# Optimization experiments

Hardware: AMD Instinct MI355X
Metric: run time of the kernel (lower is better)

Reference implementation:

```python
import jax, jax.numpy as jnp
import numpy as np

G, M, K = 4096, 50, 30          # graphs, nodes per graph, sort-pool k
H, NUM_LAYERS, F_IN = 32, 3, 128
DEG = 8
N = G * M
E = N * DEG
D_LAT = H * NUM_LAYERS + 1       # 97 = conv1d kernel/stride
DENSE_DIM = (((K - 2) // 2 + 1) - 5 + 1) * 32  # 352


def setup_inputs() -> dict:
    key = jax.random.key(0)
    ks = jax.random.split(key, 14)
    x = jax.random.normal(ks[0], (N, F_IN), dtype=jnp.float32)
    # graph-local random edges so each subgraph is self-contained
    offs = (jnp.arange(E, dtype=jnp.int32) // (M * DEG)) * M
    src = jax.random.randint(ks[1], (E,), 0, M, dtype=jnp.int32) + offs
    dst = jax.random.randint(ks[2], (E,), 0, M, dtype=jnp.int32) + offs
    edge_index = jnp.stack([src, dst])
    batch = jnp.repeat(jnp.arange(G, dtype=jnp.int32), M)

    def lin(k, i, o):
        return (jax.random.normal(k, (i, o), dtype=jnp.float32) / np.sqrt(i)).astype(jnp.float32)

    W0, b0 = lin(ks[3], F_IN, H), jnp.zeros((H,), jnp.float32)
    W1, b1 = lin(ks[4], H, H), jnp.zeros((H,), jnp.float32)
    W2, b2 = lin(ks[5], H, H), jnp.zeros((H,), jnp.float32)
    W3, b3 = lin(ks[6], H, 1), jnp.zeros((1,), jnp.float32)
    C1w = (jax.random.normal(ks[7], (16, 1, D_LAT)) / np.sqrt(D_LAT)).astype(jnp.float32)
    C1b = jnp.zeros((16,), jnp.float32)
    C2w = (jax.random.normal(ks[8], (32, 16, 5)) / np.sqrt(16 * 5)).astype(jnp.float32)
    C2b = jnp.zeros((32,), jnp.float32)
    L1w, L1b = lin(ks[9], DENSE_DIM, 128), jnp.zeros((128,), jnp.float32)
    L2w, L2b = lin(ks[10], 128, 1), jnp.zeros((1,), jnp.float32)
    return {"x": x, "edge_index": edge_index, "batch": batch,
            "W0": W0, "b0": b0, "W1": W1, "b1": b1, "W2": W2, "b2": b2,
            "W3": W3, "b3": b3, "C1w": C1w, "C1b": C1b, "C2w": C2w, "C2b": C2b,
            "L1w": L1w, "L1b": L1b, "L2w": L2w, "L2b": L2b}


def _gcn_norm(edge_index, n):
    # add self loops, symmetric normalization (PyG GCNConv default)
    loop = jnp.arange(n, dtype=edge_index.dtype)
    src = jnp.concatenate([edge_index[0], loop])
    dst = jnp.concatenate([edge_index[1], loop])
    deg = jax.ops.segment_sum(jnp.ones_like(dst, dtype=jnp.float32), dst, num_segments=n)
    dinv = jnp.where(deg > 0, deg ** -0.5, 0.0)
    return src, dst, dinv[src] * dinv[dst]


def _gcn_conv(h, W, b, src, dst, norm, n):
    h = h @ W                                    # [N, out]
    msg = h[src] * norm[:, None]                 # gather + weight
    return jax.ops.segment_sum(msg, dst, num_segments=n) + b


def reference(x, edge_index, batch, W0, b0, W1, b1, W2, b2, W3, b3,
              C1w, C1b, C2w, C2b, L1w, L1b, L2w, L2b):
    n = x.shape[0]
    src, dst, norm = _gcn_norm(edge_index, n)
    h1 = jnp.tanh(_gcn_conv(x, W0, b0, src, dst, norm, n))
    h2 = jnp.tanh(_gcn_conv(h1, W1, b1, src, dst, norm, n))
    h3 = jnp.tanh(_gcn_conv(h2, W2, b2, src, dst, norm, n))
    h4 = jnp.tanh(_gcn_conv(h3, W3, b3, src, dst, norm, n))
    lat = jnp.concatenate([h1, h2, h3, h4], axis=-1)      # [N, 97]
    # global_sort_pool: graphs are contiguous equal-size blocks (batch = arange(G).repeat(M)),
    # sort nodes within each graph by last channel, descending, keep top K
    xd = lat.reshape(G, M, D_LAT)
    order = jnp.argsort(-xd[..., -1], axis=1)             # [G, M]
    xs = jnp.take_along_axis(xd, order[..., None], axis=1)[:, :K]  # [G, K, 97]
    # Conv1d(1,16,97,stride=97) on [G,1,K*97] == per-slot linear over the 97 latent dims
    z = jnp.einsum('gtd,cd->gct', xs, C1w[:, 0, :]) + C1b[None, :, None]  # [G,16,K]
    z = jax.nn.relu(z)
    z = z.reshape(G, 16, K // 2, 2).max(axis=-1)          # MaxPool1d(2,2) -> [G,16,15]
    z = jax.lax.conv_general_dilated(z, C2w, window_strides=(1,), padding='VALID',
                                     dimension_numbers=('NCH', 'OIH', 'NCH'))
    z = jax.nn.relu(z + C2b[None, :, None])               # [G,32,11]
    z = z.reshape(G, -1)                                  # [G,352]
    z = jax.nn.relu(z @ L1w + L1b)
    # dropout: eval mode (identity)
    return z @ L2w + L2b                                  # [G,1]
```

## Files before the change

kernel.cpp:

```cpp
#include <hip/hip_runtime.h>
#include <math.h>

#define NG 4096
#define M 50
#define KTOP 30
#define H 32
#define F_IN 128
#define EPG 400
#define PADE 552
#define E_TOTAL (NG * EPG)
#define DLAT 97
#define LATS 100
#define NTHREADS 256

__device__ __forceinline__ float fast_tanh(float x) {
    x = fminf(fmaxf(x, -15.f), 15.f);
    float e = __expf(2.f * x);
    return 1.f - 2.f / (e + 1.f);
}

template <int KIN>
__device__ __forceinline__ void gcn_matmul(const float* hin, int istride,
                                           const float* __restrict__ W,
                                           float (*tb)[H], int tid) {
    const int j = tid & 31, iset = tid >> 5;
    float acc[7];
    int rows[7];
#pragma unroll
    for (int r = 0; r < 7; r++) {
        acc[r] = 0.f;
        int i = iset + r * 8;
        rows[r] = (i >= M) ? (M - 1) : i;
    }
#pragma unroll 2
    for (int k4 = 0; k4 < KIN / 4; k4++) {
        const float w0 = W[(4 * k4 + 0) * H + j];
        const float w1 = W[(4 * k4 + 1) * H + j];
        const float w2 = W[(4 * k4 + 2) * H + j];
        const float w3 = W[(4 * k4 + 3) * H + j];
#pragma unroll
        for (int r = 0; r < 7; r++) {
            const float4 xv = *(const float4*)(hin + rows[r] * istride + 4 * k4);
            acc[r] += xv.x * w0 + xv.y * w1 + xv.z * w2 + xv.w * w3;
        }
    }
#pragma unroll
    for (int r = 0; r < 7; r++) {
        int i = iset + r * 8;
        if (i < M) tb[i][j] = acc[r];
    }
}

__device__ __forceinline__ void gcn_agg(const float (*tbuf)[H], const float* __restrict__ b,
                                        float (*lat)[LATS], int col0,
                                        const float* dinv, const unsigned short* csr_off,
                                        const unsigned char* csr_src, const float* csr_nrm,
                                        int tid) {
    const int j = tid & 31, iset = tid >> 5;
    for (int i = iset; i < M; i += 8) {
        float acc = tbuf[i][j] * dinv[i] * dinv[i];
        int e0 = csr_off[i], e1 = csr_off[i + 1];
        for (int e = e0; e < e1; e += 4) {
            unsigned sp = *(const unsigned*)(csr_src + e);
            float4 nr = *(const float4*)(csr_nrm + e);
            acc += tbuf[sp & 255][j] * nr.x;
            acc += tbuf[(sp >> 8) & 255][j] * nr.y;
            acc += tbuf[(sp >> 16) & 255][j] * nr.z;
            acc += tbuf[sp >> 24][j] * nr.w;
        }
        lat[i][col0 + j] = fast_tanh(acc + b[j]);
    }
}

__global__ __launch_bounds__(NTHREADS, 4)
void dgcnn_kernel(const float* __restrict__ x, const int* __restrict__ eidx,
                  const float* __restrict__ W0, const float* __restrict__ b0,
                  const float* __restrict__ W1, const float* __restrict__ b1,
                  const float* __restrict__ W2, const float* __restrict__ b2,
                  const float* __restrict__ W3, const float* __restrict__ b3,
                  const float* __restrict__ C1w, const float* __restrict__ C1b,
                  const float* __restrict__ C2w, const float* __restrict__ C2b,
                  const float* __restrict__ L1w, const float* __restrict__ L1b,
                  const float* __restrict__ L2w, const float* __restrict__ L2b,
                  float* __restrict__ out) {
    __shared__ __align__(16) float lat[M][LATS];
    __shared__ float tbuf[M][H];
    __shared__ __align__(16) float csr_nrm[PADE];
    __shared__ unsigned char csr_src[PADE];
    __shared__ unsigned short csr_off[M + 2];
    __shared__ int   degi[M];
    __shared__ float dinv[M];
    __shared__ struct Post {
        float pbuf[16][15];
        union {
            struct { float z1[16][KTOP]; unsigned char ord[52]; } a;
            struct { float z2[352]; float d1[128]; } b;
        } u;
    } post;

    const int g = blockIdx.x;
    const int tid = threadIdx.x;
    const int nbase = g * M;
    const int ebase = g * EPG;
    const float* xg = x + (size_t)nbase * F_IN;

    if (tid < M) degi[tid] = 1;
    for (int idx = tid; idx < PADE; idx += NTHREADS) {
        csr_nrm[idx] = 0.f;
        csr_src[idx] = 0;
    }
    __syncthreads();
    for (int e = tid; e < EPG; e += NTHREADS) {
        int d = eidx[E_TOTAL + ebase + e] - nbase;
        atomicAdd(&degi[d], 1);
    }
    __syncthreads();
    if (tid < M) dinv[tid] = rsqrtf((float)degi[tid]);
    if (tid < 64) {
        int cnt  = (tid < M) ? (degi[tid] - 1) : 0;
        int cntp = (cnt + 3) & ~3;
        int incl = cntp;
#pragma unroll
        for (int off = 1; off < 64; off <<= 1) {
            int nv = __shfl_up(incl, off);
            if (tid >= off) incl += nv;
        }
        if (tid < M) {
            csr_off[tid] = (unsigned short)(incl - cntp);
            degi[tid] = incl - cntp;
        }
        if (tid == M - 1) csr_off[M] = (unsigned short)incl;
    }
    __syncthreads();
    for (int e = tid; e < EPG; e += NTHREADS) {
        int s = eidx[ebase + e] - nbase;
        int d = eidx[E_TOTAL + ebase + e] - nbase;
        float nr = dinv[s] * dinv[d];
        int pos = atomicAdd(&degi[d], 1);
        csr_src[pos] = (unsigned char)s;
        csr_nrm[pos] = nr;
    }
    __syncthreads();

    gcn_matmul<F_IN>(xg, F_IN, W0, tbuf, tid);
    __syncthreads();
    gcn_agg(tbuf, b0, lat, 0, dinv, csr_off, csr_src, csr_nrm, tid);
    __syncthreads();
    gcn_matmul<H>(&lat[0][0], LATS, W1, tbuf, tid);
    __syncthreads();
    gcn_agg(tbuf, b1, lat, 32, dinv, csr_off, csr_src, csr_nrm, tid);
    __syncthreads();
    gcn_matmul<H>(&lat[0][32], LATS, W2, tbuf, tid);
    __syncthreads();
    gcn_agg(tbuf, b2, lat, 64, dinv, csr_off, csr_src, csr_nrm, tid);
    __syncthreads();
    if (tid < M) {
        float acc = 0.f;
        for (int k = 0; k < H; k++) acc += lat[tid][64 + k] * W3[k];
        tbuf[tid][0] = acc;
    }
    __syncthreads();
    if (tid < M) {
        float acc = tbuf[tid][0] * dinv[tid] * dinv[tid];
        int e0 = csr_off[tid], e1 = csr_off[tid + 1];
        for (int e = e0; e < e1; e += 4) {
            unsigned sp = *(const unsigned*)(csr_src + e);
            float4 nr = *(const float4*)(csr_nrm + e);
            acc += tbuf[sp & 255][0] * nr.x + tbuf[(sp >> 8) & 255][0] * nr.y
                 + tbuf[(sp >> 16) & 255][0] * nr.z + tbuf[sp >> 24][0] * nr.w;
        }
        lat[tid][96] = tanhf(acc + b3[0]);
    }
    __syncthreads();

    if (tid < M) {
        float v = lat[tid][96];
        int r = 0;
        for (int jj = 0; jj < M; jj++) {
            float vj = lat[jj][96];
            r += (vj > v) || (vj == v && jj < tid);
        }
        post.u.a.ord[r] = (unsigned char)tid;
    }
    __syncthreads();

    for (int idx = tid; idx < 16 * KTOP; idx += NTHREADS) {
        int t = idx >> 4, c = idx & 15;
        const float* row = lat[post.u.a.ord[t]];
        float acc = 0.f;
        for (int d = 0; d < DLAT; d++) acc += row[d] * C1w[c * DLAT + d];
        acc += C1b[c];
        post.u.a.z1[c][t] = fmaxf(acc, 0.f);
    }
    __syncthreads();

    for (int idx = tid; idx < 16 * 15; idx += NTHREADS) {
        int c = idx / 15, t = idx - c * 15;
        post.pbuf[c][t] = fmaxf(post.u.a.z1[c][2 * t], post.u.a.z1[c][2 * t + 1]);
    }
    __syncthreads();

    for (int idx = tid; idx < 352; idx += NTHREADS) {
        int o = idx / 11, t = idx - o * 11;
        float acc = C2b[o];
        for (int i = 0; i < 16; i++) {
#pragma unroll
            for (int k = 0; k < 5; k++)
                acc += post.pbuf[i][t + k] * C2w[(o * 16 + i) * 5 + k];
        }
        post.u.b.z2[idx] = fmaxf(acc, 0.f);
    }
    __syncthreads();

    if (tid < 128) {
        float acc = L1b[tid];
        for (int f = 0; f < 352; f++) acc += post.u.b.z2[f] * L1w[f * 128 + tid];
        post.u.b.d1[tid] = fmaxf(acc, 0.f);
    }
    __syncthreads();

    if (tid < 64) {
        float v = post.u.b.d1[tid] * L2w[tid]
                + post.u.b.d1[tid + 64] * L2w[tid + 64];
#pragma unroll
        for (int off = 32; off >= 1; off >>= 1)
            v += __shfl_down(v, off);
        if (tid == 0) out[g] = v + L2b[0];
    }
}

extern "C" void kernel_launch(void* const* d_in, const int* in_sizes, int n_in,
                              void* d_out, int out_size, void* d_ws, size_t ws_size,
                              hipStream_t stream) {
    const float* x    = (const float*)d_in[0];
    const int*   eidx = (const int*)d_in[1];
    dgcnn_kernel<<<NG, NTHREADS, 0, stream>>>(
        x, eidx,
        (const float*)d_in[3],  (const float*)d_in[4],
        (const float*)d_in[5],  (const float*)d_in[6],
        (const float*)d_in[7],  (const float*)d_in[8],
        (const float*)d_in[9],  (const float*)d_in[10],
        (const float*)d_in[11], (const float*)d_in[12],
        (const float*)d_in[13], (const float*)d_in[14],
        (const float*)d_in[15], (const float*)d_in[16],
        (const float*)d_in[17], (const float*)d_in[18],
        (float*)d_out);
}
```

Baseline: 425.7 us.

## Pre-transpose weights into workspace for vectorized loads and split dense layer

Adds a small prep kernel that transposes W0/W1/W2 and L1w and pads C1w to 100 columns in the workspace, so the main kernel can read weights as float4 rows. The conv1 dot product, the GCN matmuls and the dense layer now use float4 loads from both shared memory and global memory. The dense layer is split across all 256 threads as two halves that are then reduced, and L2 is folded into that reduction. tbuf is overlapped in a union with the post-processing buffers to save shared memory. The cost is an extra kernel launch per call, and the lat padding columns must be zeroed.

```diff
diff --git a/kernel.cpp b/kernel.cpp
--- a/kernel.cpp
+++ b/kernel.cpp
@@ -13,17 +13,49 @@
 #define LATS 100
 #define NTHREADS 256
 
+#define WS_WT0 0
+#define WS_WT1 4096
+#define WS_WT2 5120
+#define WS_C1P 6144
+#define WS_L1T 7744
+#define WS_TOTAL 52800
+
 __device__ __forceinline__ float fast_tanh(float x) {
     x = fminf(fmaxf(x, -15.f), 15.f);
     float e = __expf(2.f * x);
     return 1.f - 2.f / (e + 1.f);
 }
 
+__global__ void prep_kernel(const float* __restrict__ W0, const float* __restrict__ W1,
+                            const float* __restrict__ W2, const float* __restrict__ C1w,
+                            const float* __restrict__ L1w, float* __restrict__ ws) {
+    const int tid = blockIdx.x * blockDim.x + threadIdx.x;
+    const int nthr = gridDim.x * blockDim.x;
+    for (int idx = tid; idx < 4096; idx += nthr) {
+        int j = idx >> 7, k = idx & 127;
+        ws[WS_WT0 + idx] = W0[k * 32 + j];
+    }
+    for (int idx = tid; idx < 1024; idx += nthr) {
+        int j = idx >> 5, k = idx & 31;
+        ws[WS_WT1 + idx] = W1[k * 32 + j];
+        ws[WS_WT2 + idx] = W2[k * 32 + j];
+    }
+    for (int idx = tid; idx < 1600; idx += nthr) {
+        int c = idx / 100, d = idx - c * 100;
+        ws[WS_C1P + idx] = (d < DLAT) ? C1w[c * DLAT + d] : 0.f;
+    }
+    for (int idx = tid; idx < 45056; idx += nthr) {
+        int j = idx / 352, f = idx - j * 352;
+        ws[WS_L1T + idx] = L1w[f * 128 + j];
+    }
+}
+
 template <int KIN>
 __device__ __forceinline__ void gcn_matmul(const float* hin, int istride,
-                                           const float* __restrict__ W,
+                                           const float* __restrict__ Wt,
                                            float (*tb)[H], int tid) {
     const int j = tid & 31, iset = tid >> 5;
+    const float* wrow = Wt + j * KIN;
     float acc[7];
     int rows[7];
 #pragma unroll
@@ -34,14 +66,11 @@
     }
 #pragma unroll 2
     for (int k4 = 0; k4 < KIN / 4; k4++) {
-        const float w0 = W[(4 * k4 + 0) * H + j];
-        const float w1 = W[(4 * k4 + 1) * H + j];
-        const float w2 = W[(4 * k4 + 2) * H + j];
-        const float w3 = W[(4 * k4 + 3) * H + j];
+        const float4 wv = *(const float4*)(wrow + 4 * k4);
 #pragma unroll
         for (int r = 0; r < 7; r++) {
             const float4 xv = *(const float4*)(hin + rows[r] * istride + 4 * k4);
-            acc[r] += xv.x * w0 + xv.y * w1 + xv.z * w2 + xv.w * w3;
+            acc[r] += xv.x * wv.x + xv.y * wv.y + xv.z * wv.z + xv.w * wv.w;
         }
     }
 #pragma unroll
@@ -74,29 +103,31 @@
 
 __global__ __launch_bounds__(NTHREADS, 4)
 void dgcnn_kernel(const float* __restrict__ x, const int* __restrict__ eidx,
-                  const float* __restrict__ W0, const float* __restrict__ b0,
-                  const float* __restrict__ W1, const float* __restrict__ b1,
-                  const float* __restrict__ W2, const float* __restrict__ b2,
+                  const float* __restrict__ ws,
+                  const float* __restrict__ b0, const float* __restrict__ b1,
+                  const float* __restrict__ b2,
                   const float* __restrict__ W3, const float* __restrict__ b3,
-                  const float* __restrict__ C1w, const float* __restrict__ C1b,
+                  const float* __restrict__ C1b,
                   const float* __restrict__ C2w, const float* __restrict__ C2b,
-                  const float* __restrict__ L1w, const float* __restrict__ L1b,
+                  const float* __restrict__ L1b,
                   const float* __restrict__ L2w, const float* __restrict__ L2b,
                   float* __restrict__ out) {
     __shared__ __align__(16) float lat[M][LATS];
-    __shared__ float tbuf[M][H];
+    __shared__ __align__(16) union TU {
+        float tbuf[M][H];
+        struct {
+            float pbuf[16][15];
+            union {
+                struct { float z1[16][KTOP]; unsigned char ord[52]; } a;
+                struct { float z2[352]; float red[256]; } b;
+            } u;
+        } post;
+    } tu;
     __shared__ __align__(16) float csr_nrm[PADE];
     __shared__ unsigned char csr_src[PADE];
     __shared__ unsigned short csr_off[M + 2];
     __shared__ int   degi[M];
     __shared__ float dinv[M];
-    __shared__ struct Post {
-        float pbuf[16][15];
-        union {
-            struct { float z1[16][KTOP]; unsigned char ord[52]; } a;
-            struct { float z2[352]; float d1[128]; } b;
-        } u;
-    } post;
 
     const int g = blockIdx.x;
     const int tid = threadIdx.x;
@@ -109,6 +140,7 @@
         csr_nrm[idx] = 0.f;
         csr_src[idx] = 0;
     }
+    if (tid < 3 * M) lat[tid / 3][DLAT + tid % 3] = 0.f;
     __syncthreads();
     for (int e = tid; e < EPG; e += NTHREADS) {
         int d = eidx[E_TOTAL + ebase + e] - nbase;
@@ -142,32 +174,32 @@
     }
     __syncthreads();
 
-    gcn_matmul<F_IN>(xg, F_IN, W0, tbuf, tid);
-    __syncthreads();
-    gcn_agg(tbuf, b0, lat, 0, dinv, csr_off, csr_src, csr_nrm, tid);
-    __syncthreads();
-    gcn_matmul<H>(&lat[0][0], LATS, W1, tbuf, tid);
-    __syncthreads();
-    gcn_agg(tbuf, b1, lat, 32, dinv, csr_off, csr_src, csr_nrm, tid);
-    __syncthreads();
-    gcn_matmul<H>(&lat[0][32], LATS, W2, tbuf, tid);
-    __syncthreads();
-    gcn_agg(tbuf, b2, lat, 64, dinv, csr_off, csr_src, csr_nrm, tid);
+    gcn_matmul<F_IN>(xg, F_IN, ws + WS_WT0, tu.tbuf, tid);
+    __syncthreads();
+    gcn_agg(tu.tbuf, b0, lat, 0, dinv, csr_off, csr_src, csr_nrm, tid);
+    __syncthreads();
+    gcn_matmul<H>(&lat[0][0], LATS, ws + WS_WT1, tu.tbuf, tid);
+    __syncthreads();
+    gcn_agg(tu.tbuf, b1, lat, 32, dinv, csr_off, csr_src, csr_nrm, tid);
+    __syncthreads();
+    gcn_matmul<H>(&lat[0][32], LATS, ws + WS_WT2, tu.tbuf, tid);
+    __syncthreads();
+    gcn_agg(tu.tbuf, b2, lat, 64, dinv, csr_off, csr_src, csr_nrm, tid);
     __syncthreads();
     if (tid < M) {
         float acc = 0.f;
         for (int k = 0; k < H; k++) acc += lat[tid][64 + k] * W3[k];
-        tbuf[tid][0] = acc;
+        tu.tbuf[tid][0] = acc;
     }
     __syncthreads();
     if (tid < M) {
-        float acc = tbuf[tid][0] * dinv[tid] * dinv[tid];
+        float acc = tu.tbuf[tid][0] * dinv[tid] * dinv[tid];
         int e0 = csr_off[tid], e1 = csr_off[tid + 1];
         for (int e = e0; e < e1; e += 4) {
             unsigned sp = *(const unsigned*)(csr_src + e);
             float4 nr = *(const float4*)(csr_nrm + e);
-            acc += tbuf[sp & 255][0] * nr.x + tbuf[(sp >> 8) & 255][0] * nr.y
-                 + tbuf[(sp >> 16) & 255][0] * nr.z + tbuf[sp >> 24][0] * nr.w;
+            acc += tu.tbuf[sp & 255][0] * nr.x + tu.tbuf[(sp >> 8) & 255][0] * nr.y
+                 + tu.tbuf[(sp >> 16) & 255][0] * nr.z + tu.tbuf[sp >> 24][0] * nr.w;
         }
         lat[tid][96] = tanhf(acc + b3[0]);
     }
@@ -180,23 +212,28 @@
             float vj = lat[jj][96];
             r += (vj > v) || (vj == v && jj < tid);
         }
-        post.u.a.ord[r] = (unsigned char)tid;
+        tu.post.u.a.ord[r] = (unsigned char)tid;
     }
     __syncthreads();
 
     for (int idx = tid; idx < 16 * KTOP; idx += NTHREADS) {
         int t = idx >> 4, c = idx & 15;
-        const float* row = lat[post.u.a.ord[t]];
+        const float4* row = (const float4*)lat[tu.post.u.a.ord[t]];
+        const float4* cw  = (const float4*)(ws + WS_C1P + c * LATS);
         float acc = 0.f;
-        for (int d = 0; d < DLAT; d++) acc += row[d] * C1w[c * DLAT + d];
-        acc += C1b[c];
-        post.u.a.z1[c][t] = fmaxf(acc, 0.f);
+#pragma unroll 5
+        for (int q = 0; q < LATS / 4; q++) {
+            float4 rv = row[q], wv = cw[q];
+            acc += rv.x * wv.x + rv.y * wv.y + rv.z * wv.z + rv.w * wv.w;
+        }
+        tu.post.u.a.z1[c][t] = fmaxf(acc + C1b[c], 0.f);
     }
     __syncthreads();
 
     for (int idx = tid; idx < 16 * 15; idx += NTHREADS) {
         int c = idx / 15, t = idx - c * 15;
-        post.pbuf[c][t] = fmaxf(post.u.a.z1[c][2 * t], post.u.a.z1[c][2 * t + 1]);
+        tu.post.pbuf[c][t] = fmaxf(tu.post.u.a.z1[c][2 * t],
+                                   tu.post.u.a.z1[c][2 * t + 1]);
     }
     __syncthreads();
 
@@ -206,22 +243,31 @@
         for (int i = 0; i < 16; i++) {
 #pragma unroll
             for (int k = 0; k < 5; k++)
-                acc += post.pbuf[i][t + k] * C2w[(o * 16 + i) * 5 + k];
-        }
-        post.u.b.z2[idx] = fmaxf(acc, 0.f);
-    }
-    __syncthreads();
-
-    if (tid < 128) {
-        float acc = L1b[tid];
-        for (int f = 0; f < 352; f++) acc += post.u.b.z2[f] * L1w[f * 128 + tid];
-        post.u.b.d1[tid] = fmaxf(acc, 0.f);
-    }
-    __syncthreads();
-
+                acc += tu.post.pbuf[i][t + k] * C2w[(o * 16 + i) * 5 + k];
+        }
+        tu.post.u.b.z2[idx] = fmaxf(acc, 0.f);
+    }
+    __syncthreads();
+
+    {
+        int jj = tid & 127, half = tid >> 7;
+        const float4* lw = (const float4*)(ws + WS_L1T + jj * 352 + half * 176);
+        const float4* zz = (const float4*)(tu.post.u.b.z2 + half * 176);
+        float acc = (half == 0) ? L1b[jj] : 0.f;
+#pragma unroll 4
+        for (int q = 0; q < 44; q++) {
+            float4 zv = zz[q], wv = lw[q];
+            acc += zv.x * wv.x + zv.y * wv.y + zv.z * wv.z + zv.w * wv.w;
+        }
+        tu.post.u.b.red[tid] = acc;
+    }
+    __syncthreads();
+    if (tid < 128)
+        tu.post.u.b.red[tid] = fmaxf(tu.post.u.b.red[tid] + tu.post.u.b.red[tid + 128],
+                                     0.f) * L2w[tid];
+    __syncthreads();
     if (tid < 64) {
-        float v = post.u.b.d1[tid] * L2w[tid]
-                + post.u.b.d1[tid + 64] * L2w[tid + 64];
+        float v = tu.post.u.b.red[tid] + tu.post.u.b.red[tid + 64];
 #pragma unroll
         for (int off = 32; off >= 1; off >>= 1)
             v += __shfl_down(v, off);
@@ -234,15 +280,19 @@
                               hipStream_t stream) {
     const float* x    = (const float*)d_in[0];
     const int*   eidx = (const int*)d_in[1];
+    float* ws = (float*)d_ws;
+    prep_kernel<<<64, 256, 0, stream>>>(
+        (const float*)d_in[3],  (const float*)d_in[5],
+        (const float*)d_in[7],  (const float*)d_in[11],
+        (const float*)d_in[15], ws);
     dgcnn_kernel<<<NG, NTHREADS, 0, stream>>>(
-        x, eidx,
-        (const float*)d_in[3],  (const float*)d_in[4],
-        (const float*)d_in[5],  (const float*)d_in[6],
-        (const float*)d_in[7],  (const float*)d_in[8],
+        x, eidx, ws,
+        (const float*)d_in[4],  (const float*)d_in[6],
+        (const float*)d_in[8],
         (const float*)d_in[9],  (const float*)d_in[10],
-        (const float*)d_in[11], (const float*)d_in[12],
+        (const float*)d_in[12],
         (const float*)d_in[13], (const float*)d_in[14],
-        (const float*)d_in[15], (const float*)d_in[16],
+        (const float*)d_in[16],
         (const float*)d_in[17], (const float*)d_in[18],
         (float*)d_out);
 }
```

New measurement: 488.9 us. 14.9% more time.

## Overlap first GCN matmul with CSR build and software-pipeline row loads

Applied to the files above, without the earlier changes.

The first-layer matmul over x is moved up so it runs between the degree-count atomics and the CSR construction. Its global loads then overlap with edge processing instead of waiting behind two extra barriers. Inside gcn_matmul, the float4 row loads for the next k-step are prefetched into registers while the current step computes (double buffering). The launch bound is lowered from 4 to 3 blocks per SM so the extra registers fit, which risks lower occupancy.

```diff
diff --git a/kernel.cpp b/kernel.cpp
--- a/kernel.cpp
+++ b/kernel.cpp
@@ -24,25 +24,42 @@
                                            const float* __restrict__ W,
                                            float (*tb)[H], int tid) {
     const int j = tid & 31, iset = tid >> 5;
+    const float* base[7];
     float acc[7];
-    int rows[7];
 #pragma unroll
     for (int r = 0; r < 7; r++) {
         acc[r] = 0.f;
         int i = iset + r * 8;
-        rows[r] = (i >= M) ? (M - 1) : i;
-    }
+        base[r] = hin + ((i >= M) ? (M - 1) : i) * istride;
+    }
+    float4 cur[7];
+#pragma unroll
+    for (int r = 0; r < 7; r++) cur[r] = *(const float4*)(base[r]);
 #pragma unroll 2
-    for (int k4 = 0; k4 < KIN / 4; k4++) {
+    for (int k4 = 0; k4 < KIN / 4 - 1; k4++) {
+        float4 nxt[7];
+#pragma unroll
+        for (int r = 0; r < 7; r++)
+            nxt[r] = *(const float4*)(base[r] + 4 * (k4 + 1));
         const float w0 = W[(4 * k4 + 0) * H + j];
         const float w1 = W[(4 * k4 + 1) * H + j];
         const float w2 = W[(4 * k4 + 2) * H + j];
         const float w3 = W[(4 * k4 + 3) * H + j];
 #pragma unroll
-        for (int r = 0; r < 7; r++) {
-            const float4 xv = *(const float4*)(hin + rows[r] * istride + 4 * k4);
-            acc[r] += xv.x * w0 + xv.y * w1 + xv.z * w2 + xv.w * w3;
-        }
+        for (int r = 0; r < 7; r++)
+            acc[r] += cur[r].x * w0 + cur[r].y * w1 + cur[r].z * w2 + cur[r].w * w3;
+#pragma unroll
+        for (int r = 0; r < 7; r++) cur[r] = nxt[r];
+    }
+    {
+        const int k4 = KIN / 4 - 1;
+        const float w0 = W[(4 * k4 + 0) * H + j];
+        const float w1 = W[(4 * k4 + 1) * H + j];
+        const float w2 = W[(4 * k4 + 2) * H + j];
+        const float w3 = W[(4 * k4 + 3) * H + j];
+#pragma unroll
+        for (int r = 0; r < 7; r++)
+            acc[r] += cur[r].x * w0 + cur[r].y * w1 + cur[r].z * w2 + cur[r].w * w3;
     }
 #pragma unroll
     for (int r = 0; r < 7; r++) {
@@ -72,7 +89,7 @@
     }
 }
 
-__global__ __launch_bounds__(NTHREADS, 4)
+__global__ __launch_bounds__(NTHREADS, 3)
 void dgcnn_kernel(const float* __restrict__ x, const int* __restrict__ eidx,
                   const float* __restrict__ W0, const float* __restrict__ b0,
                   const float* __restrict__ W1, const float* __restrict__ b1,
@@ -84,13 +101,13 @@
                   const float* __restrict__ L2w, const float* __restrict__ L2b,
                   float* __restrict__ out) {
     __shared__ __align__(16) float lat[M][LATS];
-    __shared__ float tbuf[M][H];
+    __shared__ __align__(16) float tbuf[M][H];
     __shared__ __align__(16) float csr_nrm[PADE];
     __shared__ unsigned char csr_src[PADE];
     __shared__ unsigned short csr_off[M + 2];
     __shared__ int   degi[M];
     __shared__ float dinv[M];
-    __shared__ struct Post {
+    __shared__ __align__(16) struct Post {
         float pbuf[16][15];
         union {
             struct { float z1[16][KTOP]; unsigned char ord[52]; } a;
@@ -114,6 +131,7 @@
         int d = eidx[E_TOTAL + ebase + e] - nbase;
         atomicAdd(&degi[d], 1);
     }
+    gcn_matmul<F_IN>(xg, F_IN, W0, tbuf, tid);
     __syncthreads();
     if (tid < M) dinv[tid] = rsqrtf((float)degi[tid]);
     if (tid < 64) {
@@ -142,8 +160,6 @@
     }
     __syncthreads();
 
-    gcn_matmul<F_IN>(xg, F_IN, W0, tbuf, tid);
-    __syncthreads();
     gcn_agg(tbuf, b0, lat, 0, dinv, csr_off, csr_src, csr_nrm, tid);
     __syncthreads();
     gcn_matmul<H>(&lat[0][0], LATS, W1, tbuf, tid);
```

Measured after the change: 437.0 us. 1.03x slower.
